# Kernel tuning notes

Hardware: AMD Instinct MI355X
Metric: run time of the kernel (lower is better)

## Reference

```python
import math
import jax, jax.numpy as jnp
import numpy as np

L_LAYERS, H, D, DV, DM, LMAX, V = 4, 16, 1024, 64, 4096, 1024, 32000


def setup_inputs() -> dict:
    key = jax.random.key(0)
    ks = iter(jax.random.split(key, 40))
    def rn(shape, s=0.02):
        return jax.random.normal(next(ks), shape, jnp.float32) * s
    x_ids = jax.random.randint(next(ks), (LMAX,), 0, V)
    return dict(
        x_ids=x_ids,
        word_emb=rn((V, D)), pos_emb=rn((LMAX, D)),
        Wq=rn((L_LAYERS, H, D, D)), bq=jnp.zeros((L_LAYERS, H, D), jnp.float32),
        Wk=rn((L_LAYERS, H, D, D)), bk=jnp.zeros((L_LAYERS, H, D), jnp.float32),
        Wv=rn((L_LAYERS, H, D, DV)), bv=jnp.zeros((L_LAYERS, H, DV), jnp.float32),
        Wo=rn((L_LAYERS, H * DV, D)), bo=jnp.zeros((L_LAYERS, D), jnp.float32),
        g1=rn((L_LAYERS, D), 0.01), b1=rn((L_LAYERS, D), 0.01),
        g2=rn((L_LAYERS, D), 0.01), b2=rn((L_LAYERS, D), 0.01),
        W1=rn((L_LAYERS, D, DM)), bm1=jnp.zeros((L_LAYERS, DM), jnp.float32),
        W2=rn((L_LAYERS, DM, D)), bm2=jnp.zeros((L_LAYERS, D), jnp.float32),
        gf=rn((D,), 0.01), bf=rn((D,), 0.01),
        Wu=rn((D, V)), bu=jnp.zeros((V,), jnp.float32),
    )


def _ln(x, g, b):
    # original normalizes each row over the full embedding vector (biased std)
    mu = jnp.mean(x, axis=-1, keepdims=True)
    sd = jnp.sqrt(jnp.mean((x - mu) ** 2, axis=-1, keepdims=True))
    return g * (x - mu) / sd + b


def reference(x_ids, word_emb, pos_emb, Wq, bq, Wk, bk, Wv, bv, Wo, bo,
              g1, b1, g2, b2, W1, bm1, W2, bm2, gf, bf, Wu, bu):
    x = word_emb[x_ids] + pos_emb[jnp.arange(LMAX)]          # (LMAX, D)
    mask = jnp.tril(jnp.ones((LMAX, LMAX), bool))
    scale = 1.0 / math.sqrt(D)                               # d_attn = d_e
    for l in range(L_LAYERS):
        xn = _ln(x, g1[l], b1[l])
        q = jnp.einsum('ld,hde->hle', xn, Wq[l]) + bq[l][:, None, :]
        k = jnp.einsum('ld,hde->hle', xn, Wk[l]) + bk[l][:, None, :]
        v = jnp.einsum('ld,hdv->hlv', xn, Wv[l]) + bv[l][:, None, :]
        s = jnp.einsum('hqe,hke->hqk', q, k)                 # (H, LMAX, LMAX)
        s = jnp.where(mask, s, -jnp.inf)
        a = jax.nn.softmax(s * scale, axis=-1)
        o = jnp.einsum('hqk,hkv->hqv', a, v)                 # (H, LMAX, DV)
        # faithful reproduction of MHAttention's OVERLAPPING slice writes:
        # head h writes columns [h, h+DV), later heads overwrite earlier ones
        y = jnp.zeros((LMAX, H * DV), x.dtype)
        for h in range(H):
            y = y.at[:, h:h + DV].set(o[h])
        x = x + y @ Wo[l] + bo[l]
        xn2 = _ln(x, g2[l], b2[l])
        # x + act_layer(xn2) where act_layer(z) = z + mlp2(gelu(mlp1(z)))
        x = x + xn2 + jax.nn.gelu(xn2 @ W1[l] + bm1[l]) @ W2[l] + bm2[l]
    x = _ln(x, gf, bf)
    return jax.nn.softmax(x @ Wu + bu, axis=-1)              # (LMAX, V)
```

## Files before the change

### kernel.cpp

```cpp
#include <hip/hip_runtime.h>

typedef __bf16 bf16_t;
typedef __bf16 bf16x8 __attribute__((ext_vector_type(8)));
typedef float f32x4 __attribute__((ext_vector_type(4)));
typedef unsigned int u32;

#define SEQ    1024
#define DEMB   1024
#define NHEAD  16
#define DVDIM  64
#define DMLP   4096
#define NVOCAB 32000
#define NLAYER 4

typedef const __attribute__((address_space(1))) void gas_t;
typedef __attribute__((address_space(3))) void las_t;

__device__ __forceinline__ void gload_lds16(const void* g, void* l) {
  __builtin_amdgcn_global_load_lds((gas_t*)g, (las_t*)l, 16, 0, 0);
}

union PackU { bf16_t h[2]; u32 u; };
union B4U  { uint2 u; bf16_t h[4]; };

__device__ __forceinline__ float blockSum(float v, float* red) {
  #pragma unroll
  for (int o = 32; o > 0; o >>= 1) v += __shfl_down(v, o, 64);
  __syncthreads();
  if ((threadIdx.x & 63) == 0) red[threadIdx.x >> 6] = v;
  __syncthreads();
  return (red[0] + red[1]) + (red[2] + red[3]);
}
__device__ __forceinline__ float blockMax(float v, float* red) {
  #pragma unroll
  for (int o = 32; o > 0; o >>= 1) v = fmaxf(v, __shfl_down(v, o, 64));
  __syncthreads();
  if ((threadIdx.x & 63) == 0) red[threadIdx.x >> 6] = v;
  __syncthreads();
  return fmaxf(fmaxf(red[0], red[1]), fmaxf(red[2], red[3]));
}

__device__ __forceinline__ void ln_body(float4 v, const float* __restrict__ g,
                                        const float* __restrict__ b,
                                        bf16_t* __restrict__ xn, int row, int t,
                                        float* red, float* xupd_row) {
  float mu = blockSum(v.x + v.y + v.z + v.w, red) * (1.0f / DEMB);
  float dx = v.x - mu, dy = v.y - mu, dz = v.z - mu, dw = v.w - mu;
  float var = blockSum(dx * dx + dy * dy + dz * dz + dw * dw, red) * (1.0f / DEMB);
  float inv = 1.0f / sqrtf(var);
  float4 gv = *(const float4*)(g + t * 4);
  float4 bv = *(const float4*)(b + t * 4);
  float o0 = gv.x * dx * inv + bv.x;
  float o1 = gv.y * dy * inv + bv.y;
  float o2 = gv.z * dz * inv + bv.z;
  float o3 = gv.w * dw * inv + bv.w;
  PackU p0, p1;
  p0.h[0] = (bf16_t)o0; p0.h[1] = (bf16_t)o1;
  p1.h[0] = (bf16_t)o2; p1.h[1] = (bf16_t)o3;
  uint2 st; st.x = p0.u; st.y = p1.u;
  *(uint2*)(xn + (long)row * DEMB + t * 4) = st;
  if (xupd_row) {
    float4 nv; nv.x = v.x + o0; nv.y = v.y + o1; nv.z = v.z + o2; nv.w = v.w + o3;
    *(float4*)(xupd_row + t * 4) = nv;
  }
}

__global__ void __launch_bounds__(256)
embedln_k(const int* __restrict__ ids, const float* __restrict__ we,
          const float* __restrict__ pe, const float* __restrict__ g,
          const float* __restrict__ b, float* __restrict__ x,
          bf16_t* __restrict__ xn) {
  __shared__ float red[4];
  const int row = blockIdx.x, t = threadIdx.x;
  const long id = ids[row];
  float4 a = *(const float4*)(we + id * (long)DEMB + t * 4);
  float4 p = *(const float4*)(pe + (long)row * DEMB + t * 4);
  float4 v; v.x = a.x + p.x; v.y = a.y + p.y; v.z = a.z + p.z; v.w = a.w + p.w;
  *(float4*)(x + (long)row * DEMB + t * 4) = v;
  ln_body(v, g, b, xn, row, t, red, nullptr);
}

__global__ void __launch_bounds__(256)
ln_k(const float* __restrict__ x, const float* __restrict__ g,
     const float* __restrict__ b, bf16_t* __restrict__ xn,
     float* __restrict__ xupd) {
  __shared__ float red[4];
  const int row = blockIdx.x, t = threadIdx.x;
  float4 v = *(const float4*)(x + (long)row * DEMB + t * 4);
  ln_body(v, g, b, xn, row, t, red, xupd ? xupd + (long)row * DEMB : nullptr);
}

__global__ void __launch_bounds__(256)
redln_k(const float* __restrict__ P, const float* __restrict__ bm2,
        float* __restrict__ X, const float* __restrict__ g,
        const float* __restrict__ b, bf16_t* __restrict__ xn) {
  __shared__ float red[4];
  const int row = blockIdx.x, t = threadIdx.x;
  const long i = (long)row * 1024 + t * 4;
  float4 x = *(float4*)(X + i);
  #pragma unroll
  for (int z = 0; z < 4; ++z) {
    float4 p = *(const float4*)(P + (long)z * 1048576 + i);
    x.x += p.x; x.y += p.y; x.z += p.z; x.w += p.w;
  }
  float4 bb = *(const float4*)(bm2 + t * 4);
  x.x += bb.x; x.y += bb.y; x.z += bb.z; x.w += bb.w;
  *(float4*)(X + i) = x;
  ln_body(x, g, b, xn, row, t, red, nullptr);
}

__global__ void biascat_k(const float* __restrict__ bq, const float* __restrict__ bk,
                          float* __restrict__ out) {
  const int z = blockIdx.x, t = threadIdx.x;
  const int l = z >> 5, i = z & 31;
  const float* src = (i < NHEAD) ? (bq + (long)(l * NHEAD + i) * DEMB)
                                 : (bk + (long)(l * NHEAD + i - NHEAD) * DEMB);
  *(float4*)(out + (long)z * DEMB + t * 4) = *(const float4*)(src + t * 4);
}

__global__ void zyb_k(bf16_t* __restrict__ y) {
  *(uint4*)((char*)y + ((long)blockIdx.x * 256 + threadIdx.x) * 16) = uint4{0, 0, 0, 0};
}

__device__ __forceinline__ void tconv_tile(const float* __restrict__ ip,
                                           bf16_t* __restrict__ op,
                                           int R, int C, int rx, int ry,
                                           float (*tf)[65]) {
  const int c0 = rx * 64, r0 = ry * 64;
  const int t = threadIdx.x;
  const int lr = t >> 4, lc = (t & 15) * 4;
  #pragma unroll
  for (int p = 0; p < 4; ++p) {
    const float4 v = *(const float4*)(ip + (long)(r0 + lr + 16 * p) * C + (c0 + lc));
    tf[lr + 16 * p][lc + 0] = v.x;
    tf[lr + 16 * p][lc + 1] = v.y;
    tf[lr + 16 * p][lc + 2] = v.z;
    tf[lr + 16 * p][lc + 3] = v.w;
  }
  __syncthreads();
  const int j = t & 7;
  const int n = t >> 3;
  #pragma unroll
  for (int p = 0; p < 2; ++p) {
    const int nn = n + 32 * p;
    u32 w[4];
    #pragma unroll
    for (int q = 0; q < 4; ++q) {
      PackU u;
      u.h[0] = (bf16_t)tf[j * 8 + 2 * q][nn];
      u.h[1] = (bf16_t)tf[j * 8 + 2 * q + 1][nn];
      w[q] = u.u;
    }
    *(uint4*)(op + (long)(c0 + nn) * R + (r0 + j * 8)) = *(uint4*)&w[0];
  }
}

__global__ void __launch_bounds__(256)
tconvall_k(const float* __restrict__ Wq, const float* __restrict__ Wk,
           const float* __restrict__ Wv, const float* __restrict__ Wo,
           const float* __restrict__ W1, const float* __restrict__ W2,
           const float* __restrict__ Wu,
           bf16_t* __restrict__ WTqk, bf16_t* __restrict__ WTv,
           bf16_t* __restrict__ WTo, bf16_t* __restrict__ WT1,
           bf16_t* __restrict__ WT2, bf16_t* __restrict__ WTu) {
  __shared__ float tf[64][65];
  const long DD = (long)DEMB * DEMB;
  const int b = blockIdx.x;
  const float* ip; bf16_t* op; int R, C, rx, ry;
  if (b < 32768) {
    const int z = b >> 8, rem = b & 255; ry = rem >> 4; rx = rem & 15;
    R = 1024; C = 1024;
    const int l = z >> 5, i = z & 31;
    ip = (i < NHEAD) ? (Wq + (long)(l * NHEAD + i) * DD)
                     : (Wk + (long)(l * NHEAD + i - NHEAD) * DD);
    op = WTqk + (long)z * DD;
  } else if (b < 33792) {
    const int idx = b - 32768; const int z = idx >> 4; ry = idx & 15; rx = 0;
    R = 1024; C = 64;
    ip = Wv + (long)z * 65536; op = WTv + (long)z * 65536;
  } else if (b < 33920) {
    const int idx = b - 33792; const int z = idx >> 5; ry = (idx >> 4) & 1; rx = idx & 15;
    R = 128; C = 1024;
    ip = Wo + (long)z * DD; op = WTo + (long)z * 131072;
  } else if (b < 38016) {
    const int idx = b - 33920; const int z = idx >> 10; ry = (idx >> 6) & 15; rx = idx & 63;
    R = 1024; C = 4096;
    ip = W1 + (long)z * 4194304; op = WT1 + (long)z * 4194304;
  } else if (b < 42112) {
    const int idx = b - 38016; const int z = idx >> 10; ry = (idx >> 4) & 63; rx = idx & 15;
    R = 4096; C = 1024;
    ip = W2 + (long)z * 4194304; op = WT2 + (long)z * 4194304;
  } else {
    const int idx = b - 42112; ry = idx / 500; rx = idx - ry * 500;
    R = 1024; C = 32000;
    ip = Wu; op = WTu;
  }
  tconv_tile(ip, op, R, C, rx, ry, tf);
}

template<int MODE, int BN, bool CAUSAL, bool TRIMK>
__global__ void __launch_bounds__(256)
gemm_k(const bf16_t* __restrict__ A, const bf16_t* __restrict__ B,
       const float* __restrict__ bias, void* __restrict__ Cv,
       int M, int N, int K, int lda, int ldb,
       long aB, long bB, long cB, int biasB) {
  __shared__ bf16_t lsA[128 * 32];
  __shared__ bf16_t lsB[BN * 32];

  const int t = threadIdx.x;
  const int bz = blockIdx.z;
  const int m0 = blockIdx.y * 128;
  const int n0 = blockIdx.x * BN;
  if (CAUSAL && n0 > m0 + 127) return;

  const bf16_t* Ap = A + (long)bz * aB;
  const bf16_t* Bp = B + (long)bz * bB;
  const int kEnd = TRIMK ? min(K, m0 + 128) : K;

  constexpr int NS = BN / 32;
  const int lane = t & 63;
  const int wid = t >> 6;
  const int wr = (wid >> 1) * 64;
  const int wc = (wid & 1) * (BN / 2);
  const int fr = lane & 15, fg = lane >> 4;
  const int srow = lane >> 2;
  const int skc  = (lane & 3) * 8;

  f32x4 acc[4][NS] = {};

  for (int k0 = 0; k0 < kEnd; k0 += 32) {
    if (k0) __syncthreads();
    #pragma unroll
    for (int i = 0; i < 2; ++i) {
      const int seg = wid * 2 + i;
      gload_lds16(Ap + (long)(m0 + seg * 16 + srow) * lda + (k0 + skc),
                  lsA + seg * 512);
    }
    if (BN == 128) {
      #pragma unroll
      for (int i = 0; i < 2; ++i) {
        const int seg = wid * 2 + i;
        gload_lds16(Bp + (long)(n0 + seg * 16 + srow) * ldb + (k0 + skc),
                    lsB + seg * 512);
      }
    } else {
      gload_lds16(Bp + (long)(n0 + wid * 16 + srow) * ldb + (k0 + skc),
                  lsB + wid * 512);
    }
    __syncthreads();

    bf16x8 af[4], bfv[NS];
    #pragma unroll
    for (int ms = 0; ms < 4; ++ms)
      af[ms] = *(const bf16x8*)(lsA + (wr + ms * 16 + fr) * 32 + fg * 8);
    #pragma unroll
    for (int ns = 0; ns < NS; ++ns)
      bfv[ns] = *(const bf16x8*)(lsB + (wc + ns * 16 + fr) * 32 + fg * 8);
    #pragma unroll
    for (int ms = 0; ms < 4; ++ms)
      #pragma unroll
      for (int ns = 0; ns < NS; ++ns)
        acc[ms][ns] = __builtin_amdgcn_mfma_f32_16x16x32_bf16(
            af[ms], bfv[ns], acc[ms][ns], 0, 0, 0);
  }

  #pragma unroll
  for (int ms = 0; ms < 4; ++ms) {
    #pragma unroll
    for (int ns = 0; ns < NS; ++ns) {
      const int col = n0 + wc + ns * 16 + fr;
      const float bvv = bias ? bias[(long)bz * biasB + col] : 0.0f;
      #pragma unroll
      for (int r = 0; r < 4; ++r) {
        const int row = m0 + wr + ms * 16 + fg * 4 + r;
        float v = acc[ms][ns][r] + bvv;
        if (MODE == 1) {
          ((float*)Cv)[(long)bz * cB + (long)row * N + col] += v;
        } else if (MODE == 2) {
          ((float*)Cv)[(long)bz * cB + (long)row * N + col] = v;
        } else if (MODE == 3) {
          float gl = 0.5f * v * (1.0f + tanhf(0.7978845608028654f * (v + 0.044715f * v * v * v)));
          ((bf16_t*)Cv)[(long)bz * cB + (long)row * N + col] = (bf16_t)gl;
        } else {
          if (bz == NHEAD - 1) {
            ((bf16_t*)Cv)[(long)row * 128 + (NHEAD - 1) + col] = (bf16_t)v;
          } else if (col == 0) {
            ((bf16_t*)Cv)[(long)row * 128 + bz] = (bf16_t)v;
          }
        }
      }
    }
  }
}

#define GPHASE(buf, mh, nh, STAGE, VM) do {                                            \
  bf16x8 af[4][2], bfv[2][2];                                                          \
  _Pragma("unroll") for (int mf = 0; mf < 4; ++mf) {                                   \
    const int r = wm * 128 + ((mh) * 4 + mf) * 16 + (lane & 15);                       \
    _Pragma("unroll") for (int ks = 0; ks < 2; ++ks) {                                 \
      const int slot = ks * 4 + (lane >> 4);                                           \
      af[mf][ks] = *(const bf16x8*)(lds + (buf) * 32768 + r * 64 +                     \
                                    ((slot ^ (r & 7)) << 3)); } }                      \
  _Pragma("unroll") for (int nf = 0; nf < 2; ++nf) {                                   \
    const int r = wn * 64 + ((nh) * 2 + nf) * 16 + (lane & 15);                        \
    _Pragma("unroll") for (int ks = 0; ks < 2; ++ks) {                                 \
      const int slot = ks * 4 + (lane >> 4);                                           \
      bfv[nf][ks] = *(const bf16x8*)(lds + (buf) * 32768 + 16384 + r * 64 +            \
                                     ((slot ^ (r & 7)) << 3)); } }                     \
  STAGE;                                                                               \
  __builtin_amdgcn_s_barrier();                                                        \
  asm volatile("s_waitcnt lgkmcnt(0)" ::: "memory");                                   \
  __builtin_amdgcn_sched_barrier(0);                                                   \
  __builtin_amdgcn_s_setprio(1);                                                       \
  _Pragma("unroll") for (int mf = 0; mf < 4; ++mf)                                     \
    _Pragma("unroll") for (int nf = 0; nf < 2; ++nf)                                   \
      _Pragma("unroll") for (int ks = 0; ks < 2; ++ks)                                 \
        acc[(mh) * 4 + mf][(nh) * 2 + nf] = __builtin_amdgcn_mfma_f32_16x16x32_bf16(   \
            af[mf][ks], bfv[nf][ks], acc[(mh) * 4 + mf][(nh) * 2 + nf], 0, 0, 0);      \
  __builtin_amdgcn_s_setprio(0);                                                       \
  VM;                                                                                  \
  __builtin_amdgcn_s_barrier();                                                        \
} while (0)

template<int MODE, bool CAUSAL, bool HASV>
__global__ void __launch_bounds__(512, 1)
gemm256_k(const bf16_t* __restrict__ A, const bf16_t* __restrict__ B,
          const float* __restrict__ bias, void* __restrict__ Cv,
          int M, int N, int K, long aB, long bB, long cB, int biasB,
          const bf16_t* __restrict__ B2, const float* __restrict__ bias2,
          bf16_t* __restrict__ Cv2) {
  __shared__ bf16_t lds[65536];

  const int t = threadIdx.x;
  const int lane = t & 63, w = t >> 6;
  const int wm = w >> 2, wn = w & 3;
  const int bz = blockIdx.z;
  const int m0 = blockIdx.y * 256, n0 = blockIdx.x * 256;
  if (CAUSAL && n0 > m0 + 255) return;

  const bool vm = HASV && (bz == 32);
  const bf16_t* Ap = A + (long)bz * aB;
  const bf16_t* Bp = vm ? B2 : B + (long)bz * bB;
  const int NT = K >> 6;

  f32x4 acc[8][4] = {};

  auto stA = [&](int half, int kt, int buf) {
    #pragma unroll
    for (int rr = 0; rr < 2; ++rr) {
      const int rw0 = rr * 64 + w * 8;
      const int row0 = ((rw0 >> 6) << 7) | (half << 6) | (rw0 & 63);
      const int r = row0 + (lane >> 3);
      const int slot = lane & 7;
      gload_lds16(Ap + (long)(m0 + r) * K + (kt << 6) + ((slot ^ (r & 7)) << 3),
                  lds + buf * 32768 + row0 * 64);
    }
  };
  auto stB = [&](int half, int kt, int buf) {
    #pragma unroll
    for (int rr = 0; rr < 2; ++rr) {
      const int rw0 = rr * 64 + w * 8;
      const int row0 = ((rw0 >> 5) << 6) | (half << 5) | (rw0 & 31);
      const int r = row0 + (lane >> 3);
      const int slot = lane & 7;
      gload_lds16(Bp + (long)(n0 + r) * K + (kt << 6) + ((slot ^ (r & 7)) << 3),
                  lds + buf * 32768 + 16384 + row0 * 64);
    }
  };

  stB(0, 0, 0); stA(0, 0, 0); stA(1, 0, 0); stB(1, 0, 0);
  stB(0, 1, 1); stA(0, 1, 1);
  asm volatile("s_waitcnt vmcnt(4)" ::: "memory");
  __builtin_amdgcn_s_barrier();

  for (int it = 0; it < (NT >> 1); ++it) {
    const int tt = it * 2;
    const int s1 = min(tt + 1, NT - 1);
    const int s2 = min(tt + 2, NT - 1);
    const int s3 = min(tt + 3, NT - 1);
    GPHASE(0, 0, 0, { stA(1, s1, 1); }, );
    GPHASE(0, 1, 0, { stB(1, s1, 1); }, );
    GPHASE(0, 0, 1, { stB(0, s2, 0); }, );
    GPHASE(0, 1, 1, { stA(0, s2, 0); }, asm volatile("s_waitcnt vmcnt(4)" ::: "memory"));
    GPHASE(1, 0, 0, { stA(1, s2, 0); }, );
    GPHASE(1, 1, 0, { stB(1, s2, 0); }, );
    GPHASE(1, 0, 1, { stB(0, s3, 1); }, );
    GPHASE(1, 1, 1, { stA(0, s3, 1); }, asm volatile("s_waitcnt vmcnt(4)" ::: "memory"));
  }
  asm volatile("s_waitcnt vmcnt(0)" ::: "memory");

  #pragma unroll
  for (int mf = 0; mf < 8; ++mf) {
    #pragma unroll
    for (int nf = 0; nf < 4; ++nf) {
      const int col = n0 + wn * 64 + nf * 16 + (lane & 15);
      const int row0 = m0 + wm * 128 + mf * 16 + (lane >> 4) * 4;
      if (HASV && vm) {
        const float bvv = bias2[col];
        PackU p0, p1;
        p0.h[0] = (bf16_t)(acc[mf][nf][0] + bvv);
        p0.h[1] = (bf16_t)(acc[mf][nf][1] + bvv);
        p1.h[0] = (bf16_t)(acc[mf][nf][2] + bvv);
        p1.h[1] = (bf16_t)(acc[mf][nf][3] + bvv);
        uint2 st; st.x = p0.u; st.y = p1.u;
        *(uint2*)(Cv2 + (long)col * M + row0) = st;
      } else {
        const float bvv = bias ? bias[(long)bz * biasB + col] : 0.0f;
        #pragma unroll
        for (int r = 0; r < 4; ++r) {
          const float v = acc[mf][nf][r] + bvv;
          if (MODE == 0)
            ((bf16_t*)Cv)[(long)bz * cB + (long)(row0 + r) * N + col] = (bf16_t)v;
          else
            ((float*)Cv)[(long)bz * cB + (long)(row0 + r) * N + col] = v;
        }
      }
    }
  }
}

__global__ void __launch_bounds__(256)
smax_k(bf16_t* __restrict__ s) {
  __shared__ float red[4];
  const int q = blockIdx.x, h = blockIdx.y, t = threadIdx.x;
  bf16_t* sr = s + ((long)h * SEQ + q) * SEQ;
  const int L = q + 1;
  const float scale = 0.03125f;
  B4U b; b.u = *(const uint2*)(sr + t * 4);
  float x[4];
  float m = -1e30f;
  #pragma unroll
  for (int j = 0; j < 4; ++j) {
    x[j] = (float)b.h[j] * scale;
    if (t * 4 + j < L) m = fmaxf(m, x[j]);
  }
  m = blockMax(m, red);
  float e[4], sum = 0.0f;
  #pragma unroll
  for (int j = 0; j < 4; ++j) {
    e[j] = (t * 4 + j < L) ? expf(x[j] - m) : 0.0f;
    sum += e[j];
  }
  __syncthreads();
  sum = blockSum(sum, red);
  const float inv = 1.0f / sum;
  #pragma unroll
  for (int j = 0; j < 4; ++j) b.h[j] = (bf16_t)(e[j] * inv);
  *(uint2*)(sr + t * 4) = b.u;
}

__global__ void __launch_bounds__(1024)
vsmax_k(float* __restrict__ out) {
  __shared__ float rm[16], rs[16];
  const int row = blockIdx.x, t = threadIdx.x;
  float* r = out + (long)row * NVOCAB;
  float v[32];
  const int nlast = (t < NVOCAB - 31 * 1024) ? 32 : 31;
  float m = -1e30f;
  #pragma unroll
  for (int j = 0; j < 31; ++j) { v[j] = r[j * 1024 + t]; m = fmaxf(m, v[j]); }
  if (nlast == 32) { v[31] = r[31 * 1024 + t]; m = fmaxf(m, v[31]); } else v[31] = -1e30f;
  float s = 0.0f;
  #pragma unroll
  for (int j = 0; j < 32; ++j) s += expf(v[j] - m);
  #pragma unroll
  for (int o = 32; o > 0; o >>= 1) {
    const float mo = __shfl_down(m, o, 64);
    const float so = __shfl_down(s, o, 64);
    const float M2 = fmaxf(m, mo);
    s = s * expf(m - M2) + so * expf(mo - M2);
    m = M2;
  }
  if ((t & 63) == 0) { rm[t >> 6] = m; rs[t >> 6] = s; }
  __syncthreads();
  float M = -1e30f;
  #pragma unroll
  for (int i = 0; i < 16; ++i) M = fmaxf(M, rm[i]);
  float S = 0.0f;
  #pragma unroll
  for (int i = 0; i < 16; ++i) S += rs[i] * expf(rm[i] - M);
  const float inv = 1.0f / S;
  #pragma unroll
  for (int j = 0; j < 31; ++j) r[j * 1024 + t] = expf(v[j] - M) * inv;
  if (nlast == 32) r[31 * 1024 + t] = expf(v[31] - M) * inv;
}

extern "C" void kernel_launch(void* const* d_in, const int* in_sizes, int n_in,
                              void* d_out, int out_size, void* d_ws, size_t ws_size,
                              hipStream_t stream) {
  (void)in_sizes; (void)n_in; (void)out_size; (void)ws_size;
  const int*   x_ids = (const int*)  d_in[0];
  const float* wemb  = (const float*)d_in[1];
  const float* pemb  = (const float*)d_in[2];
  const float* Wq    = (const float*)d_in[3];
  const float* bq    = (const float*)d_in[4];
  const float* Wk    = (const float*)d_in[5];
  const float* bk    = (const float*)d_in[6];
  const float* Wv    = (const float*)d_in[7];
  const float* bv    = (const float*)d_in[8];
  const float* Wo    = (const float*)d_in[9];
  const float* bo    = (const float*)d_in[10];
  const float* g1    = (const float*)d_in[11];
  const float* b1    = (const float*)d_in[12];
  const float* g2    = (const float*)d_in[13];
  const float* b2    = (const float*)d_in[14];
  const float* W1    = (const float*)d_in[15];
  const float* bm1   = (const float*)d_in[16];
  const float* W2    = (const float*)d_in[17];
  const float* bm2   = (const float*)d_in[18];
  const float* gf    = (const float*)d_in[19];
  const float* bfin  = (const float*)d_in[20];
  const float* Wu    = (const float*)d_in[21];
  const float* bu    = (const float*)d_in[22];

  char* ws = (char*)d_ws;
  float*  X    = (float*) ws;
  bf16_t* ACT  = (bf16_t*)(ws + (4u   << 20));
  bf16_t* VbT  = (bf16_t*)(ws + (6u   << 20));
  bf16_t* Yb   = (bf16_t*)(ws + (10u  << 20));
  bf16_t* H1   = (bf16_t*)(ws + (12u  << 20));
  bf16_t* QKb  = (bf16_t*)(ws + (20u  << 20));
  float*  PART = (float*) (ws + (84u  << 20));
  float*  BIAS = (float*) (ws + (100u << 20));
  bf16_t* WTqk = (bf16_t*)(ws + (128u << 20));
  bf16_t* WTv  = (bf16_t*)(ws + (384u << 20));
  bf16_t* WTo  = (bf16_t*)(ws + (392u << 20));
  bf16_t* WT1  = (bf16_t*)(ws + (400u << 20));
  bf16_t* WT2  = (bf16_t*)(ws + (432u << 20));
  bf16_t* WTu  = (bf16_t*)(ws + (464u << 20));

  bf16_t* Sb  = (bf16_t*)d_out;
  float*  OUT = (float*)d_out;

  const long DD = (long)DEMB * DEMB;
  const long SD = (long)SEQ * DEMB;

  embedln_k<<<SEQ, 256, 0, stream>>>(x_ids, wemb, pemb, g1, b1, X, ACT);
  biascat_k<<<128, 256, 0, stream>>>(bq, bk, BIAS);
  zyb_k<<<64, 256, 0, stream>>>(Yb);
  tconvall_k<<<50112, 256, 0, stream>>>(Wq, Wk, Wv, Wo, W1, W2, Wu,
                                        WTqk, WTv, WTo, WT1, WT2, WTu);

  for (int l = 0; l < NLAYER; ++l) {
    gemm256_k<0, false, true><<<dim3(4, 4, 33), 512, 0, stream>>>(
        ACT, WTqk + (long)l * 32 * DD, BIAS + (long)l * 32 * DEMB, QKb,
        SEQ, DEMB, DEMB, 0L, DD, SD, DEMB,
        WTv + (long)l * DD, bv + (long)l * NHEAD * DVDIM, VbT);

    gemm256_k<0, true, false><<<dim3(4, 4, NHEAD), 512, 0, stream>>>(
        QKb, QKb + (long)NHEAD * SD, nullptr, Sb,
        SEQ, SEQ, DEMB, SD, SD, (long)SEQ * SEQ, 0, nullptr, nullptr, nullptr);
    smax_k<<<dim3(SEQ, NHEAD), 256, 0, stream>>>(Sb);

    gemm_k<6, 64, false, true><<<dim3(1, 8, NHEAD), 256, 0, stream>>>(
        Sb, VbT, nullptr, Yb,
        SEQ, DVDIM, SEQ, SEQ, SEQ, (long)SEQ * SEQ, (long)DVDIM * SEQ, 0L, 0);

    gemm_k<1, 128, false, false><<<dim3(8, 8, 1), 256, 0, stream>>>(
        Yb, WTo + (long)l * DEMB * 128, bo + (long)l * DEMB, X,
        SEQ, DEMB, 128, 128, 128, 0L, 0L, 0L, 0);

    ln_k<<<SEQ, 256, 0, stream>>>(X, g2 + l * DEMB, b2 + l * DEMB, ACT, X);

    gemm_k<3, 128, false, false><<<dim3(32, 8, 1), 256, 0, stream>>>(
        ACT, WT1 + (long)l * DMLP * DEMB, bm1 + (long)l * DMLP, H1,
        SEQ, DMLP, DEMB, DEMB, DEMB, 0L, 0L, 0L, 0);
    gemm_k<2, 128, false, false><<<dim3(8, 8, 4), 256, 0, stream>>>(
        H1, WT2 + (long)l * DEMB * DMLP, nullptr, PART,
        SEQ, DEMB, 1024, DMLP, DMLP, 1024L, 1024L, (long)SEQ * DEMB, 0);
    if (l < NLAYER - 1)
      redln_k<<<SEQ, 256, 0, stream>>>(PART, bm2 + (long)l * DEMB, X,
                                       g1 + (l + 1) * DEMB, b1 + (l + 1) * DEMB, ACT);
    else
      redln_k<<<SEQ, 256, 0, stream>>>(PART, bm2 + (long)l * DEMB, X, gf, bfin, ACT);
  }

  gemm256_k<2, false, false><<<dim3(125, 4, 1), 512, 0, stream>>>(
      ACT, WTu, bu, OUT, SEQ, NVOCAB, DEMB, 0L, 0L, 0L, 0,
      nullptr, nullptr, nullptr);
  vsmax_k<<<SEQ, 1024, 0, stream>>>(OUT);
}
```

Baseline: 1.540 ms.

## Widen weight transpose tiles, split V projection, use GEMV for surviving head columns

The weight transpose-convert kernel now handles 64x256 tiles per block instead of 64x64, so it launches about a quarter as many blocks. The V projection moves out of the fused 256-tile QK GEMM into its own 128-tile GEMM with a transposed bf16 store. Attention-times-V for heads 0..14 is replaced by a per-row dot-product kernel that computes only the single output column that survives the overlapping writes. Only the last head runs a full GEMM. This cuts the wasted P·V work and the block-scheduling overhead, at the cost of an extra kernel launch and a less reused V GEMM.

Result: no change. 1.559 ms (+1.2%).

```diff
diff --git a/kernel.cpp b/kernel.cpp
--- a/kernel.cpp
+++ b/kernel.cpp
@@ -122,39 +122,6 @@
   *(uint4*)((char*)y + ((long)blockIdx.x * 256 + threadIdx.x) * 16) = uint4{0, 0, 0, 0};
 }
 
-__device__ __forceinline__ void tconv_tile(const float* __restrict__ ip,
-                                           bf16_t* __restrict__ op,
-                                           int R, int C, int rx, int ry,
-                                           float (*tf)[65]) {
-  const int c0 = rx * 64, r0 = ry * 64;
-  const int t = threadIdx.x;
-  const int lr = t >> 4, lc = (t & 15) * 4;
-  #pragma unroll
-  for (int p = 0; p < 4; ++p) {
-    const float4 v = *(const float4*)(ip + (long)(r0 + lr + 16 * p) * C + (c0 + lc));
-    tf[lr + 16 * p][lc + 0] = v.x;
-    tf[lr + 16 * p][lc + 1] = v.y;
-    tf[lr + 16 * p][lc + 2] = v.z;
-    tf[lr + 16 * p][lc + 3] = v.w;
-  }
-  __syncthreads();
-  const int j = t & 7;
-  const int n = t >> 3;
-  #pragma unroll
-  for (int p = 0; p < 2; ++p) {
-    const int nn = n + 32 * p;
-    u32 w[4];
-    #pragma unroll
-    for (int q = 0; q < 4; ++q) {
-      PackU u;
-      u.h[0] = (bf16_t)tf[j * 8 + 2 * q][nn];
-      u.h[1] = (bf16_t)tf[j * 8 + 2 * q + 1][nn];
-      w[q] = u.u;
-    }
-    *(uint4*)(op + (long)(c0 + nn) * R + (r0 + j * 8)) = *(uint4*)&w[0];
-  }
-}
-
 __global__ void __launch_bounds__(256)
 tconvall_k(const float* __restrict__ Wq, const float* __restrict__ Wk,
            const float* __restrict__ Wv, const float* __restrict__ Wo,
@@ -163,39 +130,89 @@
            bf16_t* __restrict__ WTqk, bf16_t* __restrict__ WTv,
            bf16_t* __restrict__ WTo, bf16_t* __restrict__ WT1,
            bf16_t* __restrict__ WT2, bf16_t* __restrict__ WTu) {
-  __shared__ float tf[64][65];
+  __shared__ float tf[64 * 261];
   const long DD = (long)DEMB * DEMB;
   const int b = blockIdx.x;
-  const float* ip; bf16_t* op; int R, C, rx, ry;
-  if (b < 32768) {
-    const int z = b >> 8, rem = b & 255; ry = rem >> 4; rx = rem & 15;
-    R = 1024; C = 1024;
+  const float* ip; bf16_t* op; int R, C, rx, ry, TC;
+  if (b < 8192) {
+    const int z = b >> 6, rem = b & 63; ry = rem >> 2; rx = rem & 3;
+    R = 1024; C = 1024; TC = 256;
     const int l = z >> 5, i = z & 31;
     ip = (i < NHEAD) ? (Wq + (long)(l * NHEAD + i) * DD)
                      : (Wk + (long)(l * NHEAD + i - NHEAD) * DD);
     op = WTqk + (long)z * DD;
-  } else if (b < 33792) {
-    const int idx = b - 32768; const int z = idx >> 4; ry = idx & 15; rx = 0;
-    R = 1024; C = 64;
+  } else if (b < 9216) {
+    const int idx = b - 8192; const int z = idx >> 4; ry = idx & 15; rx = 0;
+    R = 1024; C = 64; TC = 64;
     ip = Wv + (long)z * 65536; op = WTv + (long)z * 65536;
-  } else if (b < 33920) {
-    const int idx = b - 33792; const int z = idx >> 5; ry = (idx >> 4) & 1; rx = idx & 15;
-    R = 128; C = 1024;
+  } else if (b < 9248) {
+    const int idx = b - 9216; const int z = idx >> 3, rem = idx & 7;
+    ry = rem >> 2; rx = rem & 3;
+    R = 128; C = 1024; TC = 256;
     ip = Wo + (long)z * DD; op = WTo + (long)z * 131072;
-  } else if (b < 38016) {
-    const int idx = b - 33920; const int z = idx >> 10; ry = (idx >> 6) & 15; rx = idx & 63;
-    R = 1024; C = 4096;
+  } else if (b < 10272) {
+    const int idx = b - 9248; const int z = idx >> 8, rem = idx & 255;
+    ry = rem >> 4; rx = rem & 15;
+    R = 1024; C = 4096; TC = 256;
     ip = W1 + (long)z * 4194304; op = WT1 + (long)z * 4194304;
-  } else if (b < 42112) {
-    const int idx = b - 38016; const int z = idx >> 10; ry = (idx >> 4) & 63; rx = idx & 15;
-    R = 4096; C = 1024;
+  } else if (b < 11296) {
+    const int idx = b - 10272; const int z = idx >> 8, rem = idx & 255;
+    ry = rem >> 2; rx = rem & 3;
+    R = 4096; C = 1024; TC = 256;
     ip = W2 + (long)z * 4194304; op = WT2 + (long)z * 4194304;
   } else {
-    const int idx = b - 42112; ry = idx / 500; rx = idx - ry * 500;
-    R = 1024; C = 32000;
+    const int idx = b - 11296; ry = idx / 125; rx = idx - ry * 125;
+    R = 1024; C = 32000; TC = 256;
     ip = Wu; op = WTu;
   }
-  tconv_tile(ip, op, R, C, rx, ry, tf);
+  const int c0 = rx * 256, r0 = ry * 64;
+  const int t = threadIdx.x;
+  if (TC == 256) {
+    #pragma unroll
+    for (int p = 0; p < 16; ++p) {
+      const int i = p * 256 + t;
+      const int r = i >> 6, s = i & 63;
+      const float4 v = *(const float4*)(ip + (long)(r0 + r) * C + (c0 + s * 4));
+      *(float4*)&tf[r * 261 + s * 4] = v;
+    }
+    __syncthreads();
+    const int c = t;
+    #pragma unroll
+    for (int j = 0; j < 8; ++j) {
+      u32 w[4];
+      #pragma unroll
+      for (int q = 0; q < 4; ++q) {
+        PackU u;
+        u.h[0] = (bf16_t)tf[(j * 8 + 2 * q) * 261 + c];
+        u.h[1] = (bf16_t)tf[(j * 8 + 2 * q + 1) * 261 + c];
+        w[q] = u.u;
+      }
+      *(uint4*)(op + (long)(c0 + c) * R + (r0 + j * 8)) = *(uint4*)&w[0];
+    }
+  } else {
+    #pragma unroll
+    for (int p = 0; p < 4; ++p) {
+      const int i = p * 256 + t;
+      const int r = i >> 4, s = i & 15;
+      const float4 v = *(const float4*)(ip + (long)(r0 + r) * C + (c0 + s * 4));
+      *(float4*)&tf[r * 261 + s * 4] = v;
+    }
+    __syncthreads();
+    const int c = t & 63, g = t >> 6;
+    #pragma unroll
+    for (int jj = 0; jj < 2; ++jj) {
+      const int j = g * 2 + jj;
+      u32 w[4];
+      #pragma unroll
+      for (int q = 0; q < 4; ++q) {
+        PackU u;
+        u.h[0] = (bf16_t)tf[(j * 8 + 2 * q) * 261 + c];
+        u.h[1] = (bf16_t)tf[(j * 8 + 2 * q + 1) * 261 + c];
+        w[q] = u.u;
+      }
+      *(uint4*)(op + (long)(c0 + c) * R + (r0 + j * 8)) = *(uint4*)&w[0];
+    }
+  }
 }
 
 template<int MODE, int BN, bool CAUSAL, bool TRIMK>
@@ -281,12 +298,10 @@
         } else if (MODE == 3) {
           float gl = 0.5f * v * (1.0f + tanhf(0.7978845608028654f * (v + 0.044715f * v * v * v)));
           ((bf16_t*)Cv)[(long)bz * cB + (long)row * N + col] = (bf16_t)gl;
+        } else if (MODE == 4) {
+          ((bf16_t*)Cv)[(long)col * M + row] = (bf16_t)v;
         } else {
-          if (bz == NHEAD - 1) {
-            ((bf16_t*)Cv)[(long)row * 128 + (NHEAD - 1) + col] = (bf16_t)v;
-          } else if (col == 0) {
-            ((bf16_t*)Cv)[(long)row * 128 + bz] = (bf16_t)v;
-          }
+          ((bf16_t*)Cv)[(long)row * 128 + 15 + col] = (bf16_t)v;
         }
       }
     }
@@ -322,13 +337,11 @@
   __builtin_amdgcn_s_barrier();                                                        \
 } while (0)
 
-template<int MODE, bool CAUSAL, bool HASV>
+template<int MODE, bool CAUSAL>
 __global__ void __launch_bounds__(512, 1)
 gemm256_k(const bf16_t* __restrict__ A, const bf16_t* __restrict__ B,
           const float* __restrict__ bias, void* __restrict__ Cv,
-          int M, int N, int K, long aB, long bB, long cB, int biasB,
-          const bf16_t* __restrict__ B2, const float* __restrict__ bias2,
-          bf16_t* __restrict__ Cv2) {
+          int M, int N, int K, long aB, long bB, long cB, int biasB) {
   __shared__ bf16_t lds[65536];
 
   const int t = threadIdx.x;
@@ -338,9 +351,8 @@
   const int m0 = blockIdx.y * 256, n0 = blockIdx.x * 256;
   if (CAUSAL && n0 > m0 + 255) return;
 
-  const bool vm = HASV && (bz == 32);
   const bf16_t* Ap = A + (long)bz * aB;
-  const bf16_t* Bp = vm ? B2 : B + (long)bz * bB;
+  const bf16_t* Bp = B + (long)bz * bB;
   const int NT = K >> 6;
 
   f32x4 acc[8][4] = {};
@@ -395,25 +407,14 @@
     for (int nf = 0; nf < 4; ++nf) {
       const int col = n0 + wn * 64 + nf * 16 + (lane & 15);
       const int row0 = m0 + wm * 128 + mf * 16 + (lane >> 4) * 4;
-      if (HASV && vm) {
-        const float bvv = bias2[col];
-        PackU p0, p1;
-        p0.h[0] = (bf16_t)(acc[mf][nf][0] + bvv);
-        p0.h[1] = (bf16_t)(acc[mf][nf][1] + bvv);
-        p1.h[0] = (bf16_t)(acc[mf][nf][2] + bvv);
-        p1.h[1] = (bf16_t)(acc[mf][nf][3] + bvv);
-        uint2 st; st.x = p0.u; st.y = p1.u;
-        *(uint2*)(Cv2 + (long)col * M + row0) = st;
-      } else {
-        const float bvv = bias ? bias[(long)bz * biasB + col] : 0.0f;
-        #pragma unroll
-        for (int r = 0; r < 4; ++r) {
-          const float v = acc[mf][nf][r] + bvv;
-          if (MODE == 0)
-            ((bf16_t*)Cv)[(long)bz * cB + (long)(row0 + r) * N + col] = (bf16_t)v;
-          else
-            ((float*)Cv)[(long)bz * cB + (long)(row0 + r) * N + col] = v;
-        }
+      const float bvv = bias ? bias[(long)bz * biasB + col] : 0.0f;
+      #pragma unroll
+      for (int r = 0; r < 4; ++r) {
+        const float v = acc[mf][nf][r] + bvv;
+        if (MODE == 0)
+          ((bf16_t*)Cv)[(long)bz * cB + (long)(row0 + r) * N + col] = (bf16_t)v;
+        else
+          ((float*)Cv)[(long)bz * cB + (long)(row0 + r) * N + col] = v;
       }
     }
   }
@@ -447,6 +448,27 @@
   #pragma unroll
   for (int j = 0; j < 4; ++j) b.h[j] = (bf16_t)(e[j] * inv);
   *(uint2*)(sr + t * 4) = b.u;
+}
+
+__global__ void __launch_bounds__(256)
+avgemv_k(const bf16_t* __restrict__ P, const bf16_t* __restrict__ V,
+         bf16_t* __restrict__ Yb) {
+  const int wav = blockIdx.x * 4 + (threadIdx.x >> 6);
+  const int lane = threadIdx.x & 63;
+  const int h = wav >> 10, q = wav & 1023;
+  const bf16_t* pr = P + ((long)h * SEQ + q) * SEQ;
+  const bf16_t* vc = V + (long)h * 64 * SEQ;
+  float s = 0.0f;
+  #pragma unroll
+  for (int half = 0; half < 2; ++half) {
+    bf16x8 a = *(const bf16x8*)(pr + half * 512 + lane * 8);
+    bf16x8 v = *(const bf16x8*)(vc + half * 512 + lane * 8);
+    #pragma unroll
+    for (int j = 0; j < 8; ++j) s += (float)a[j] * (float)v[j];
+  }
+  #pragma unroll
+  for (int o = 32; o > 0; o >>= 1) s += __shfl_down(s, o, 64);
+  if (lane == 0) Yb[(long)q * 128 + h] = (bf16_t)s;
 }
 
 __global__ void __launch_bounds__(1024)
@@ -538,23 +560,26 @@
   embedln_k<<<SEQ, 256, 0, stream>>>(x_ids, wemb, pemb, g1, b1, X, ACT);
   biascat_k<<<128, 256, 0, stream>>>(bq, bk, BIAS);
   zyb_k<<<64, 256, 0, stream>>>(Yb);
-  tconvall_k<<<50112, 256, 0, stream>>>(Wq, Wk, Wv, Wo, W1, W2, Wu,
+  tconvall_k<<<13296, 256, 0, stream>>>(Wq, Wk, Wv, Wo, W1, W2, Wu,
                                         WTqk, WTv, WTo, WT1, WT2, WTu);
 
   for (int l = 0; l < NLAYER; ++l) {
-    gemm256_k<0, false, true><<<dim3(4, 4, 33), 512, 0, stream>>>(
+    gemm256_k<0, false><<<dim3(4, 4, 32), 512, 0, stream>>>(
         ACT, WTqk + (long)l * 32 * DD, BIAS + (long)l * 32 * DEMB, QKb,
-        SEQ, DEMB, DEMB, 0L, DD, SD, DEMB,
-        WTv + (long)l * DD, bv + (long)l * NHEAD * DVDIM, VbT);
-
-    gemm256_k<0, true, false><<<dim3(4, 4, NHEAD), 512, 0, stream>>>(
+        SEQ, DEMB, DEMB, 0L, DD, SD, DEMB);
+    gemm_k<4, 128, false, false><<<dim3(8, 8, 1), 256, 0, stream>>>(
+        ACT, WTv + (long)l * DD, bv + (long)l * NHEAD * DVDIM, VbT,
+        SEQ, NHEAD * DVDIM, DEMB, DEMB, DEMB, 0L, 0L, 0L, 0);
+
+    gemm256_k<0, true><<<dim3(4, 4, NHEAD), 512, 0, stream>>>(
         QKb, QKb + (long)NHEAD * SD, nullptr, Sb,
-        SEQ, SEQ, DEMB, SD, SD, (long)SEQ * SEQ, 0, nullptr, nullptr, nullptr);
+        SEQ, SEQ, DEMB, SD, SD, (long)SEQ * SEQ, 0);
     smax_k<<<dim3(SEQ, NHEAD), 256, 0, stream>>>(Sb);
 
-    gemm_k<6, 64, false, true><<<dim3(1, 8, NHEAD), 256, 0, stream>>>(
-        Sb, VbT, nullptr, Yb,
-        SEQ, DVDIM, SEQ, SEQ, SEQ, (long)SEQ * SEQ, (long)DVDIM * SEQ, 0L, 0);
+    avgemv_k<<<3840, 256, 0, stream>>>(Sb, VbT, Yb);
+    gemm_k<7, 64, false, true><<<dim3(1, 8, 1), 256, 0, stream>>>(
+        Sb + (long)(NHEAD - 1) * SEQ * SEQ, VbT + (long)(NHEAD - 1) * DVDIM * SEQ,
+        nullptr, Yb, SEQ, DVDIM, SEQ, SEQ, SEQ, 0L, 0L, 0L, 0);
 
     gemm_k<1, 128, false, false><<<dim3(8, 8, 1), 256, 0, stream>>>(
         Yb, WTo + (long)l * DEMB * 128, bo + (long)l * DEMB, X,
@@ -575,8 +600,7 @@
       redln_k<<<SEQ, 256, 0, stream>>>(PART, bm2 + (long)l * DEMB, X, gf, bfin, ACT);
   }
 
-  gemm256_k<2, false, false><<<dim3(125, 4, 1), 512, 0, stream>>>(
-      ACT, WTu, bu, OUT, SEQ, NVOCAB, DEMB, 0L, 0L, 0L, 0,
-      nullptr, nullptr, nullptr);
+  gemm256_k<2, false><<<dim3(125, 4, 1), 512, 0, stream>>>(
+      ACT, WTu, bu, OUT, SEQ, NVOCAB, DEMB, 0L, 0L, 0L, 0);
   vsmax_k<<<SEQ, 1024, 0, stream>>>(OUT);
 }
```
